# Performance work log

Measured on AMD Instinct MI355X. Metric: run time of the kernel, lower is better.

The kernel has to match this reference:

```python
import jax, jax.numpy as jnp
import numpy as np

W1 = W2 = W3 = 7  # window size


def _rel_pos_indices(w1, w2, w3):
    # Static relative-position index table, matching the torch buffer.
    g = np.stack(np.meshgrid(np.arange(w1), np.arange(w2), np.arange(w3), indexing='ij'))
    g = g.reshape(3, -1).T                      # (N, 3), N = w1*w2*w3
    rel = g[:, None, :] - g[None, :, :]         # (N, N, 3)
    rel[..., 0] += w1 - 1
    rel[..., 1] += w2 - 1
    rel[..., 2] += w3 - 1
    strides = np.array([(2 * w2 - 1) * (2 * w3 - 1), 2 * w3 - 1, 1])
    return jnp.asarray((rel * strides).sum(-1), dtype=jnp.int32)  # (N, N)


def setup_inputs() -> dict:
    key = jax.random.key(0)
    k1, k2, k3, k4 = jax.random.split(key, 4)
    dim, heads = 256, 8
    x = jax.random.normal(k1, (2, 4, 4, 4, W1, W2, W3, dim), dtype=jnp.float32)
    w_qkv = jax.random.normal(k2, (dim, 3 * dim), dtype=jnp.float32) * (dim ** -0.5)
    w_out = jax.random.normal(k3, (dim, dim), dtype=jnp.float32) * (dim ** -0.5)
    n_rel = (2 * W1 - 1) * (2 * W2 - 1) * (2 * W3 - 1)  # 2197
    rel_bias_table = jax.random.normal(k4, (n_rel, heads), dtype=jnp.float32) * 0.02
    return {"x": x, "w_qkv": w_qkv, "w_out": w_out, "rel_bias_table": rel_bias_table}


def reference(x, w_qkv, w_out, rel_bias_table):
    b, gx, gy, gz, w1, w2, w3, d = x.shape
    heads = rel_bias_table.shape[1]
    dh = d // heads
    scale = dh ** -0.5
    n = w1 * w2 * w3
    B = b * gx * gy * gz

    xf = x.reshape(B, n, d)
    qkv = xf @ w_qkv                             # (B, n, 3d)
    q, k, v = jnp.split(qkv, 3, axis=-1)

    def to_heads(t):
        return t.reshape(B, n, heads, dh).transpose(0, 2, 1, 3)  # (B, h, n, dh)

    q, k, v = to_heads(q), to_heads(k), to_heads(v)

    rel_idx = _rel_pos_indices(w1, w2, w3)                       # (n, n)
    bias = rel_bias_table[rel_idx].transpose(2, 0, 1)            # (h, n, n)

    logits = jnp.einsum('bhnd,bhmd->bhnm', q, k) * scale + bias[None]
    attn = jax.nn.softmax(logits, axis=-1)
    ctx = jnp.einsum('bhnm,bhmd->bhnd', attn, v)                 # (B, h, n, dh)

    out = ctx.transpose(0, 2, 1, 3).reshape(B, n, d) @ w_out     # (B, n, d)
    return out.reshape(b, gx, gy, gz, w1, w2, w3, d)
```

## Files before the change

kernel.cpp:

```cpp
#include <hip/hip_runtime.h>
#include <math.h>

using f16   = _Float16;
using f16x4 = __attribute__((ext_vector_type(4))) _Float16;
using f16x8 = __attribute__((ext_vector_type(8))) _Float16;
using f32x4 = __attribute__((ext_vector_type(4))) float;

#define NW    343
#define NWP   352
#define VTP   356
#define HEADS 8
#define MTOT  43904
#define LOG2E 1.4426950408889634f
#define QSC   (0.17677669529663687f * 1.4426950408889634f)
#define BMASK -30000.0f

typedef const __attribute__((address_space(1))) unsigned int* gp1_t;
typedef __attribute__((address_space(3))) unsigned int* lp3_t;
__device__ __forceinline__ void gload_lds16(const void* g, void* l) {
    __builtin_amdgcn_global_load_lds((gp1_t)g, (lp3_t)l, 16, 0, 0);
}

__global__ void cvt_x(const float* __restrict__ x, f16* __restrict__ xb) {
    int id = blockIdx.x * 256 + threadIdx.x;
    float4 v = *(const float4*)(x + id * 4);
    f16x4 o = { (f16)v.x, (f16)v.y, (f16)v.z, (f16)v.w };
    *(f16x4*)(xb + id * 4) = o;
}

__global__ void cvt_wT(const float* __restrict__ W, f16* __restrict__ WT,
                       int N, int scaleN, float sc) {
    int id = blockIdx.x * 256 + threadIdx.x;
    int n = id >> 8, k = id & 255;
    float v = W[k * N + n];
    if (n < scaleN) v *= sc;
    WT[n * 256 + k] = (f16)v;
}

__global__ void bias_k(const float* __restrict__ tab, f16* __restrict__ bp) {
    int id = blockIdx.x * 256 + threadIdx.x;
    int h = id / (NWP * NWP);
    int rem = id - h * NWP * NWP;
    int i = rem / NWP, j = rem - (rem / NWP) * NWP;
    float v;
    if (j >= NW) v = BMASK;
    else if (i >= NW) v = 0.f;
    else {
        int a1 = i / 49, a2 = (i / 7) % 7, a3 = i % 7;
        int b1 = j / 49, b2 = (j / 7) % 7, b3 = j % 7;
        int idx = (a1 - b1 + 6) * 169 + (a2 - b2 + 6) * 13 + (a3 - b3 + 6);
        v = tab[idx * 8 + h] * LOG2E;
    }
    bp[id] = (f16)v;
}

template<bool OUT_F32>
__launch_bounds__(256)
__global__ void gemm_k(const f16* __restrict__ A, const f16* __restrict__ Bt,
                       void* __restrict__ Cp, int N) {
    __shared__ f16 As[128 * 32];
    __shared__ f16 Bs[128 * 32];
    const int m0 = blockIdx.x * 128;
    const int n0 = blockIdx.y * 128;
    const int t = threadIdx.x;
    const int wave = t >> 6, lane = t & 63;
    const int q = lane >> 4, c = lane & 15;
    const int wm = (wave >> 1) * 64, wn = (wave & 1) * 64;
    const int r0 = t >> 2;
    const int c8 = (t & 3) * 8;

    f32x4 acc[4][4] = {};
#pragma unroll
    for (int ks = 0; ks < 256; ks += 32) {
        gload_lds16(&A[(size_t)(m0 + r0) * 256 + ks + c8],        &As[r0 * 32 + c8]);
        gload_lds16(&A[(size_t)(m0 + r0 + 64) * 256 + ks + c8],   &As[(r0 + 64) * 32 + c8]);
        gload_lds16(&Bt[(size_t)(n0 + r0) * 256 + ks + c8],       &Bs[r0 * 32 + c8]);
        gload_lds16(&Bt[(size_t)(n0 + r0 + 64) * 256 + ks + c8],  &Bs[(r0 + 64) * 32 + c8]);
        __syncthreads();
        f16x8 af[4], bf[4];
#pragma unroll
        for (int a = 0; a < 4; a++) af[a] = *(const f16x8*)&As[(wm + a * 16 + c) * 32 + q * 8];
#pragma unroll
        for (int b = 0; b < 4; b++) bf[b] = *(const f16x8*)&Bs[(wn + b * 16 + c) * 32 + q * 8];
#pragma unroll
        for (int a = 0; a < 4; a++)
#pragma unroll
            for (int b = 0; b < 4; b++)
                acc[a][b] = __builtin_amdgcn_mfma_f32_16x16x32_f16(af[a], bf[b], acc[a][b], 0, 0, 0);
        __syncthreads();
    }
#pragma unroll
    for (int a = 0; a < 4; a++)
#pragma unroll
        for (int b = 0; b < 4; b++) {
            int row0 = m0 + wm + a * 16 + q * 4;
            int col = n0 + wn + b * 16 + c;
#pragma unroll
            for (int r = 0; r < 4; r++) {
                float v = acc[a][b][r];
                if (OUT_F32) ((float*)Cp)[(size_t)(row0 + r) * N + col] = v;
                else         ((f16*)Cp)[(size_t)(row0 + r) * N + col] = (f16)v;
            }
        }
}

template<bool HASB>
__device__ __forceinline__ void attn_tiles(
    const f16* __restrict__ qkv, const f16* __restrict__ biasH,
    f16* __restrict__ ctx, const f16* Ks, const f16* Vt,
    size_t base, int w, int h, int q, int c, int ta, int tb)
{
    const int iqa = ta * 16 + c;
    const int iqb = tb * 16 + c;
    const int iqac = iqa < NW ? iqa : NW - 1;
    const int iqbc = iqb < NW ? iqb : NW - 1;
    f16x8 qfa = *(const f16x8*)&qkv[base + (size_t)iqac * 768 + h * 32 + q * 8];
    f16x8 qfb{};
    if constexpr (HASB) qfb = *(const f16x8*)&qkv[base + (size_t)iqbc * 768 + h * 32 + q * 8];
    const f16* browA = biasH + (size_t)iqa * NWP;
    const f16* browB = biasH + (size_t)iqb * NWP;

    f32x4 o0a = {0.f,0.f,0.f,0.f}, o1a = {0.f,0.f,0.f,0.f};
    f32x4 o0b = {0.f,0.f,0.f,0.f}, o1b = {0.f,0.f,0.f,0.f};
    float lsa = 0.f, lsb = 0.f;
#pragma unroll
    for (int jt = 0; jt < NWP / 16; jt++) {
        const int jb = jt * 16;
        f16x8 kf = *(const f16x8*)&Ks[(jb + c) * 32 + q * 8];
        f16x4 v0 = *(const f16x4*)&Vt[c * VTP + jb + q * 4];
        f16x4 v1 = *(const f16x4*)&Vt[(16 + c) * VTP + jb + q * 4];

        f16x4 bha = *(const f16x4*)&browA[jb + q * 4];
        f32x4 ba = { (float)bha[0], (float)bha[1], (float)bha[2], (float)bha[3] };
        f32x4 sa = __builtin_amdgcn_mfma_f32_16x16x32_f16(kf, qfa, ba, 0, 0, 0);
        float pa0 = __builtin_amdgcn_exp2f(sa[0]);
        float pa1 = __builtin_amdgcn_exp2f(sa[1]);
        float pa2 = __builtin_amdgcn_exp2f(sa[2]);
        float pa3 = __builtin_amdgcn_exp2f(sa[3]);
        lsa += (pa0 + pa1) + (pa2 + pa3);
        f16x4 pfa = { (f16)pa0, (f16)pa1, (f16)pa2, (f16)pa3 };
        o0a = __builtin_amdgcn_mfma_f32_16x16x16f16(v0, pfa, o0a, 0, 0, 0);
        o1a = __builtin_amdgcn_mfma_f32_16x16x16f16(v1, pfa, o1a, 0, 0, 0);

        if constexpr (HASB) {
            f16x4 bhb = *(const f16x4*)&browB[jb + q * 4];
            f32x4 bb = { (float)bhb[0], (float)bhb[1], (float)bhb[2], (float)bhb[3] };
            f32x4 sb = __builtin_amdgcn_mfma_f32_16x16x32_f16(kf, qfb, bb, 0, 0, 0);
            float pb0 = __builtin_amdgcn_exp2f(sb[0]);
            float pb1 = __builtin_amdgcn_exp2f(sb[1]);
            float pb2 = __builtin_amdgcn_exp2f(sb[2]);
            float pb3 = __builtin_amdgcn_exp2f(sb[3]);
            lsb += (pb0 + pb1) + (pb2 + pb3);
            f16x4 pfb = { (f16)pb0, (f16)pb1, (f16)pb2, (f16)pb3 };
            o0b = __builtin_amdgcn_mfma_f32_16x16x16f16(v0, pfb, o0b, 0, 0, 0);
            o1b = __builtin_amdgcn_mfma_f32_16x16x16f16(v1, pfb, o1b, 0, 0, 0);
        }
    }
    lsa += __shfl_xor(lsa, 16);
    lsa += __shfl_xor(lsa, 32);
    if (iqa < NW) {
        float inv = 1.f / lsa;
        size_t ob = (size_t)(w * NW + iqa) * 256 + h * 32;
        f16x4 s0 = { (f16)(o0a[0] * inv), (f16)(o0a[1] * inv),
                     (f16)(o0a[2] * inv), (f16)(o0a[3] * inv) };
        f16x4 s1 = { (f16)(o1a[0] * inv), (f16)(o1a[1] * inv),
                     (f16)(o1a[2] * inv), (f16)(o1a[3] * inv) };
        *(f16x4*)&ctx[ob + q * 4] = s0;
        *(f16x4*)&ctx[ob + 16 + q * 4] = s1;
    }
    if constexpr (HASB) {
        lsb += __shfl_xor(lsb, 16);
        lsb += __shfl_xor(lsb, 32);
        if (iqb < NW) {
            float inv = 1.f / lsb;
            size_t ob = (size_t)(w * NW + iqb) * 256 + h * 32;
            f16x4 s0 = { (f16)(o0b[0] * inv), (f16)(o0b[1] * inv),
                         (f16)(o0b[2] * inv), (f16)(o0b[3] * inv) };
            f16x4 s1 = { (f16)(o1b[0] * inv), (f16)(o1b[1] * inv),
                         (f16)(o1b[2] * inv), (f16)(o1b[3] * inv) };
            *(f16x4*)&ctx[ob + q * 4] = s0;
            *(f16x4*)&ctx[ob + 16 + q * 4] = s1;
        }
    }
}

__launch_bounds__(256, 3)
__global__ void attn_k(const f16* __restrict__ qkv, const f16* __restrict__ biasP,
                       f16* __restrict__ ctx) {
    const int w = blockIdx.x >> 3;
    const int h = blockIdx.x & 7;
    __shared__ f16 Ks[NWP * 32];
    __shared__ f16 Vt[32 * VTP];
    const int t = threadIdx.x;
    const size_t base = (size_t)(w * NW) * 768;

    for (int u = t; u < NWP * 4; u += 256) {
        int row = u >> 2, un = u & 3;
        int rc = row < NW ? row : NW - 1;
        gload_lds16(&qkv[base + (size_t)rc * 768 + 256 + h * 32 + un * 8], &Ks[u * 8]);
    }
    for (int u = t; u < NWP * 4; u += 256) {
        int row = u >> 2, un = u & 3;
        if (row < NW) {
            uint4 val = *(const uint4*)&qkv[base + (size_t)row * 768 + 512 + h * 32 + un * 8];
            const f16* pv = (const f16*)&val;
#pragma unroll
            for (int e = 0; e < 8; e++) Vt[(un * 8 + e) * VTP + row] = pv[e];
        } else {
#pragma unroll
            for (int e = 0; e < 8; e++) Vt[(un * 8 + e) * VTP + row] = (f16)0.f;
        }
    }
    __syncthreads();

    const int wave = t >> 6, lane = t & 63;
    const int q = lane >> 4, c = lane & 15;
    const f16* biasH = biasP + (size_t)h * NWP * NWP;

#pragma unroll
    for (int pass = 0; pass < 3; pass++) {
        int p = wave + 4 * pass;
        if (p < 10)
            attn_tiles<true >(qkv, biasH, ctx, Ks, Vt, base, w, h, q, c, 2 * p, 2 * p + 1);
        else
            attn_tiles<false>(qkv, biasH, ctx, Ks, Vt, base, w, h, q, c, p + 10, p + 10);
    }
}

extern "C" void kernel_launch(void* const* d_in, const int* in_sizes, int n_in,
                              void* d_out, int out_size, void* d_ws, size_t ws_size,
                              hipStream_t stream) {
    const float* x    = (const float*)d_in[0];
    const float* wqkv = (const float*)d_in[1];
    const float* wout = (const float*)d_in[2];
    const float* tab  = (const float*)d_in[3];

    char* ws = (char*)d_ws;
    size_t off = 0;
    f16*   xb     = (f16*)(ws + off);   off += (size_t)MTOT * 256 * 2;
    f16*   wqkvT  = (f16*)(ws + off);   off += (size_t)768 * 256 * 2;
    f16*   woutT  = (f16*)(ws + off);   off += (size_t)256 * 256 * 2;
    f16*   biasP  = (f16*)(ws + off);   off += (size_t)8 * NWP * NWP * 2;
    f16*   qkvb   = (f16*)(ws + off);   off += (size_t)MTOT * 768 * 2;
    f16*   ctxb   = (f16*)(ws + off);   off += (size_t)MTOT * 256 * 2;
    if (ws_size < off) return;

    cvt_x <<<MTOT * 256 / 1024, 256, 0, stream>>>(x, xb);
    cvt_wT<<<768, 256, 0, stream>>>(wqkv, wqkvT, 768, 256, QSC);
    cvt_wT<<<256, 256, 0, stream>>>(wout, woutT, 256, 0, 1.f);
    bias_k<<<8 * NWP * NWP / 256, 256, 0, stream>>>(tab, biasP);
    gemm_k<false><<<dim3(MTOT / 128, 768 / 128), 256, 0, stream>>>(xb, wqkvT, qkvb, 768);
    attn_k<<<128 * HEADS, 256, 0, stream>>>(qkvb, biasP, ctxb);
    gemm_k<true><<<dim3(MTOT / 128, 256 / 128), 256, 0, stream>>>(ctxb, woutT, d_out, 256);
}
```

Before: 207.8 us.

## Precompute exponentiated bias multiplier and remap GEMM workgroups for XCD locality

The relative-position bias is now stored as exp2(bias) and multiplied into the unnormalised probabilities in packed f16, so the QK MFMA no longer needs a converted bias accumulator. Padded key columns get a zero multiplier instead of a large negative bias. Row sums use packed conversion plus an fdot2 accumulate. The GEMM grid is flattened and tiles are remapped so consecutive tiles land on the same XCD, which is meant to improve L2 reuse. The trade-off is that p*e(bias) is computed in f16 without max subtraction, which can overflow or lose precision.

```diff
diff --git a/kernel.cpp b/kernel.cpp
--- a/kernel.cpp
+++ b/kernel.cpp
@@ -2,6 +2,7 @@
 #include <math.h>
 
 using f16   = _Float16;
+using f16x2 = __attribute__((ext_vector_type(2))) _Float16;
 using f16x4 = __attribute__((ext_vector_type(4))) _Float16;
 using f16x8 = __attribute__((ext_vector_type(8))) _Float16;
 using f32x4 = __attribute__((ext_vector_type(4))) float;
@@ -13,12 +14,24 @@
 #define MTOT  43904
 #define LOG2E 1.4426950408889634f
 #define QSC   (0.17677669529663687f * 1.4426950408889634f)
-#define BMASK -30000.0f
 
 typedef const __attribute__((address_space(1))) unsigned int* gp1_t;
 typedef __attribute__((address_space(3))) unsigned int* lp3_t;
 __device__ __forceinline__ void gload_lds16(const void* g, void* l) {
     __builtin_amdgcn_global_load_lds((gp1_t)g, (lp3_t)l, 16, 0, 0);
+}
+
+__device__ __forceinline__ f16x2 pk_cvt(float a, float b) {
+    return __builtin_bit_cast(f16x2, __builtin_amdgcn_cvt_pkrtz(a, b));
+}
+
+__device__ __forceinline__ float dot2acc(f16x2 a, float acc) {
+#if __has_builtin(__builtin_amdgcn_fdot2)
+    const f16x2 one2 = { (f16)1.f, (f16)1.f };
+    return __builtin_amdgcn_fdot2(a, one2, acc, false);
+#else
+    return acc + (float)a[0] + (float)a[1];
+#endif
 }
 
 __global__ void cvt_x(const float* __restrict__ x, f16* __restrict__ xb) {
@@ -43,13 +56,13 @@
     int rem = id - h * NWP * NWP;
     int i = rem / NWP, j = rem - (rem / NWP) * NWP;
     float v;
-    if (j >= NW) v = BMASK;
-    else if (i >= NW) v = 0.f;
+    if (j >= NW) v = 0.f;
+    else if (i >= NW) v = 1.f;
     else {
         int a1 = i / 49, a2 = (i / 7) % 7, a3 = i % 7;
         int b1 = j / 49, b2 = (j / 7) % 7, b3 = j % 7;
         int idx = (a1 - b1 + 6) * 169 + (a2 - b2 + 6) * 13 + (a3 - b3 + 6);
-        v = tab[idx * 8 + h] * LOG2E;
+        v = exp2f(tab[idx * 8 + h] * LOG2E);
     }
     bp[id] = (f16)v;
 }
@@ -57,11 +70,17 @@
 template<bool OUT_F32>
 __launch_bounds__(256)
 __global__ void gemm_k(const f16* __restrict__ A, const f16* __restrict__ Bt,
-                       void* __restrict__ Cp, int N) {
+                       void* __restrict__ Cp, int N, int NT) {
     __shared__ f16 As[128 * 32];
     __shared__ f16 Bs[128 * 32];
-    const int m0 = blockIdx.x * 128;
-    const int n0 = blockIdx.y * 128;
+    const int nwg = gridDim.x;
+    const int bid = blockIdx.x;
+    const int q8 = nwg >> 3, r8 = nwg & 7;
+    const int xcd = bid & 7, pos = bid >> 3;
+    const int wg = (xcd < r8 ? xcd * (q8 + 1) : r8 * (q8 + 1) + (xcd - r8) * q8) + pos;
+    const int mt = wg / NT, nt = wg - mt * NT;
+    const int m0 = mt * 128;
+    const int n0 = nt * 128;
     const int t = threadIdx.x;
     const int wave = t >> 6, lane = t & 63;
     const int q = lane >> 4, c = lane & 15;
@@ -106,7 +125,7 @@
 
 template<bool HASB>
 __device__ __forceinline__ void attn_tiles(
-    const f16* __restrict__ qkv, const f16* __restrict__ biasH,
+    const f16* __restrict__ qkv, const f16* __restrict__ ebH,
     f16* __restrict__ ctx, const f16* Ks, const f16* Vt,
     size_t base, int w, int h, int q, int c, int ta, int tb)
 {
@@ -117,12 +136,13 @@
     f16x8 qfa = *(const f16x8*)&qkv[base + (size_t)iqac * 768 + h * 32 + q * 8];
     f16x8 qfb{};
     if constexpr (HASB) qfb = *(const f16x8*)&qkv[base + (size_t)iqbc * 768 + h * 32 + q * 8];
-    const f16* browA = biasH + (size_t)iqa * NWP;
-    const f16* browB = biasH + (size_t)iqb * NWP;
+    const f16* browA = ebH + (size_t)iqa * NWP;
+    const f16* browB = ebH + (size_t)iqb * NWP;
 
     f32x4 o0a = {0.f,0.f,0.f,0.f}, o1a = {0.f,0.f,0.f,0.f};
     f32x4 o0b = {0.f,0.f,0.f,0.f}, o1b = {0.f,0.f,0.f,0.f};
     float lsa = 0.f, lsb = 0.f;
+    const f32x4 z = {0.f, 0.f, 0.f, 0.f};
 #pragma unroll
     for (int jt = 0; jt < NWP / 16; jt++) {
         const int jb = jt * 16;
@@ -130,28 +150,28 @@
         f16x4 v0 = *(const f16x4*)&Vt[c * VTP + jb + q * 4];
         f16x4 v1 = *(const f16x4*)&Vt[(16 + c) * VTP + jb + q * 4];
 
-        f16x4 bha = *(const f16x4*)&browA[jb + q * 4];
-        f32x4 ba = { (float)bha[0], (float)bha[1], (float)bha[2], (float)bha[3] };
-        f32x4 sa = __builtin_amdgcn_mfma_f32_16x16x32_f16(kf, qfa, ba, 0, 0, 0);
-        float pa0 = __builtin_amdgcn_exp2f(sa[0]);
-        float pa1 = __builtin_amdgcn_exp2f(sa[1]);
-        float pa2 = __builtin_amdgcn_exp2f(sa[2]);
-        float pa3 = __builtin_amdgcn_exp2f(sa[3]);
-        lsa += (pa0 + pa1) + (pa2 + pa3);
-        f16x4 pfa = { (f16)pa0, (f16)pa1, (f16)pa2, (f16)pa3 };
+        f16x4 eba = *(const f16x4*)&browA[jb + q * 4];
+        f32x4 sa = __builtin_amdgcn_mfma_f32_16x16x32_f16(kf, qfa, z, 0, 0, 0);
+        f16x2 pla = pk_cvt(__builtin_amdgcn_exp2f(sa[0]), __builtin_amdgcn_exp2f(sa[1]));
+        f16x2 pha = pk_cvt(__builtin_amdgcn_exp2f(sa[2]), __builtin_amdgcn_exp2f(sa[3]));
+        f16x2 ela = { eba[0], eba[1] }, eha = { eba[2], eba[3] };
+        pla *= ela; pha *= eha;
+        lsa = dot2acc(pla, lsa);
+        lsa = dot2acc(pha, lsa);
+        f16x4 pfa = { pla[0], pla[1], pha[0], pha[1] };
         o0a = __builtin_amdgcn_mfma_f32_16x16x16f16(v0, pfa, o0a, 0, 0, 0);
         o1a = __builtin_amdgcn_mfma_f32_16x16x16f16(v1, pfa, o1a, 0, 0, 0);
 
         if constexpr (HASB) {
-            f16x4 bhb = *(const f16x4*)&browB[jb + q * 4];
-            f32x4 bb = { (float)bhb[0], (float)bhb[1], (float)bhb[2], (float)bhb[3] };
-            f32x4 sb = __builtin_amdgcn_mfma_f32_16x16x32_f16(kf, qfb, bb, 0, 0, 0);
-            float pb0 = __builtin_amdgcn_exp2f(sb[0]);
-            float pb1 = __builtin_amdgcn_exp2f(sb[1]);
-            float pb2 = __builtin_amdgcn_exp2f(sb[2]);
-            float pb3 = __builtin_amdgcn_exp2f(sb[3]);
-            lsb += (pb0 + pb1) + (pb2 + pb3);
-            f16x4 pfb = { (f16)pb0, (f16)pb1, (f16)pb2, (f16)pb3 };
+            f16x4 ebb = *(const f16x4*)&browB[jb + q * 4];
+            f32x4 sb = __builtin_amdgcn_mfma_f32_16x16x32_f16(kf, qfb, z, 0, 0, 0);
+            f16x2 plb = pk_cvt(__builtin_amdgcn_exp2f(sb[0]), __builtin_amdgcn_exp2f(sb[1]));
+            f16x2 phb = pk_cvt(__builtin_amdgcn_exp2f(sb[2]), __builtin_amdgcn_exp2f(sb[3]));
+            f16x2 elb = { ebb[0], ebb[1] }, ehb = { ebb[2], ebb[3] };
+            plb *= elb; phb *= ehb;
+            lsb = dot2acc(plb, lsb);
+            lsb = dot2acc(phb, lsb);
+            f16x4 pfb = { plb[0], plb[1], phb[0], phb[1] };
             o0b = __builtin_amdgcn_mfma_f32_16x16x16f16(v0, pfb, o0b, 0, 0, 0);
             o1b = __builtin_amdgcn_mfma_f32_16x16x16f16(v1, pfb, o1b, 0, 0, 0);
         }
@@ -185,7 +205,7 @@
 }
 
 __launch_bounds__(256, 3)
-__global__ void attn_k(const f16* __restrict__ qkv, const f16* __restrict__ biasP,
+__global__ void attn_k(const f16* __restrict__ qkv, const f16* __restrict__ ebP,
                        f16* __restrict__ ctx) {
     const int w = blockIdx.x >> 3;
     const int h = blockIdx.x & 7;
@@ -215,15 +235,15 @@
 
     const int wave = t >> 6, lane = t & 63;
     const int q = lane >> 4, c = lane & 15;
-    const f16* biasH = biasP + (size_t)h * NWP * NWP;
+    const f16* ebH = ebP + (size_t)h * NWP * NWP;
 
 #pragma unroll
     for (int pass = 0; pass < 3; pass++) {
         int p = wave + 4 * pass;
         if (p < 10)
-            attn_tiles<true >(qkv, biasH, ctx, Ks, Vt, base, w, h, q, c, 2 * p, 2 * p + 1);
+            attn_tiles<true >(qkv, ebH, ctx, Ks, Vt, base, w, h, q, c, 2 * p, 2 * p + 1);
         else
-            attn_tiles<false>(qkv, biasH, ctx, Ks, Vt, base, w, h, q, c, p + 10, p + 10);
+            attn_tiles<false>(qkv, ebH, ctx, Ks, Vt, base, w, h, q, c, p + 10, p + 10);
     }
 }
 
@@ -240,7 +260,7 @@
     f16*   xb     = (f16*)(ws + off);   off += (size_t)MTOT * 256 * 2;
     f16*   wqkvT  = (f16*)(ws + off);   off += (size_t)768 * 256 * 2;
     f16*   woutT  = (f16*)(ws + off);   off += (size_t)256 * 256 * 2;
-    f16*   biasP  = (f16*)(ws + off);   off += (size_t)8 * NWP * NWP * 2;
+    f16*   ebP    = (f16*)(ws + off);   off += (size_t)8 * NWP * NWP * 2;
     f16*   qkvb   = (f16*)(ws + off);   off += (size_t)MTOT * 768 * 2;
     f16*   ctxb   = (f16*)(ws + off);   off += (size_t)MTOT * 256 * 2;
     if (ws_size < off) return;
@@ -248,8 +268,8 @@
     cvt_x <<<MTOT * 256 / 1024, 256, 0, stream>>>(x, xb);
     cvt_wT<<<768, 256, 0, stream>>>(wqkv, wqkvT, 768, 256, QSC);
     cvt_wT<<<256, 256, 0, stream>>>(wout, woutT, 256, 0, 1.f);
-    bias_k<<<8 * NWP * NWP / 256, 256, 0, stream>>>(tab, biasP);
-    gemm_k<false><<<dim3(MTOT / 128, 768 / 128), 256, 0, stream>>>(xb, wqkvT, qkvb, 768);
-    attn_k<<<128 * HEADS, 256, 0, stream>>>(qkvb, biasP, ctxb);
-    gemm_k<true><<<dim3(MTOT / 128, 256 / 128), 256, 0, stream>>>(ctxb, woutT, d_out, 256);
-}
+    bias_k<<<8 * NWP * NWP / 256, 256, 0, stream>>>(tab, ebP);
+    gemm_k<false><<<MTOT / 128 * 6, 256, 0, stream>>>(xb, wqkvT, qkvb, 768, 6);
+    attn_k<<<128 * HEADS, 256, 0, stream>>>(qkvb, ebP, ctxb);
+    gemm_k<true><<<MTOT / 128 * 2, 256, 0, stream>>>(ctxb, woutT, d_out, 256, 2);
+}
```

Result: faster. 194.1 us (-6.6%).
